# Kernel tuning notes

Hardware: AMD Instinct MI355X
Metric: run time of the kernel (lower is better)

The kernel has to match this reference:

```python
import jax, jax.numpy as jnp
import numpy as np

N_NODES = 100000
N_EDGES = 1200000
D_IN = 64
D_OUT = 32
BN_EPS = 1e-5


def setup_inputs() -> dict:
    key = jax.random.key(0)
    ks = jax.random.split(key, 8)
    x = jax.random.normal(ks[0], (N_NODES, D_IN), dtype=jnp.float32)
    edge_index = jax.random.randint(ks[1], (2, N_EDGES), 0, N_NODES, dtype=jnp.int64)
    W1s = jax.random.normal(ks[2], (3, D_IN, D_IN), dtype=jnp.float32) * 0.05
    b1s = jax.random.normal(ks[3], (3, D_IN), dtype=jnp.float32) * 0.05
    W2s = jax.random.normal(ks[4], (3, D_IN, D_IN), dtype=jnp.float32) * 0.05
    b2s = jax.random.normal(ks[5], (3, D_IN), dtype=jnp.float32) * 0.05
    gammas = jnp.ones((3, D_IN), dtype=jnp.float32)
    betas = jnp.zeros((3, D_IN), dtype=jnp.float32)
    epss = jnp.zeros((3,), dtype=jnp.float32)  # GINConv train_eps init value 0
    lin_w = jax.random.normal(ks[6], (D_IN, D_OUT), dtype=jnp.float32) * 0.05
    lin_b = jnp.zeros((D_OUT,), dtype=jnp.float32)
    return {"x": x, "edge_index": edge_index, "W1s": W1s, "b1s": b1s,
            "W2s": W2s, "b2s": b2s, "gammas": gammas, "betas": betas,
            "epss": epss, "lin_w": lin_w, "lin_b": lin_b}


def reference(x, edge_index, W1s, b1s, W2s, b2s, gammas, betas, epss, lin_w, lin_b):
    # PyG GINConv (source_to_target): out_i = nn((1+eps)*x_i + sum_{j->i} x_j)
    src = edge_index[0]
    dst = edge_index[1]
    n = x.shape[0]
    h = x
    for i in range(3):
        agg = jax.ops.segment_sum(h[src], dst, num_segments=n)  # [N, d]
        z = (1.0 + epss[i]) * h + agg
        z = jax.nn.relu(z @ W1s[i] + b1s[i])
        z = jax.nn.relu(z @ W2s[i] + b2s[i])
        # BatchNorm1d, training mode (batch statistics, biased variance)
        mu = jnp.mean(z, axis=0)
        var = jnp.var(z, axis=0)
        z = gammas[i] * (z - mu) * jax.lax.rsqrt(var + BN_EPS) + betas[i]
        h = jax.nn.relu(z)  # F.relu after each conv
    return h @ lin_w + lin_b  # [N, D_OUT]
```

## Files before the change

### kernel.cpp

```cpp
#include <hip/hip_runtime.h>
#include <hip/hip_fp16.h>

#define NBMAX 256
#define BCAP  8192
#define CHB   3584

typedef _Float16 half8 __attribute__((ext_vector_type(8)));
typedef float f32x4 __attribute__((ext_vector_type(4)));

__device__ __forceinline__ unsigned short f2h(float f) {
    __half h = __float2half_rn(f);
    return *(unsigned short*)&h;
}

__device__ __forceinline__ int scan256(int v, int* wsum, int* woff) {
    int t = threadIdx.x, lane = t & 63, wv = t >> 6;
    int x = v;
    #pragma unroll
    for (int d = 1; d < 64; d <<= 1) {
        int y = __shfl_up(x, d, 64);
        if (lane >= d) x += y;
    }
    if (lane == 63) wsum[wv] = x;
    __syncthreads();
    if (t == 0) {
        int a = 0;
        #pragma unroll
        for (int i = 0; i < 4; ++i) { woff[i] = a; a += wsum[i]; }
    }
    __syncthreads();
    return x - v + woff[wv];
}

__global__ __launch_bounds__(256) void gin_init(const void* __restrict__ edge,
                                                int* __restrict__ flag,
                                                int* __restrict__ gcount, int nb,
                                                float* __restrict__ stats, int E) {
    int t = threadIdx.x;
    for (int i = t; i < nb; i += 256) gcount[i] = 0;
    for (int i = t; i < 384; i += 256) stats[i] = 0.f;
    if (t == 0) {
        const int* p = (const int*)edge;
        int is64 = 1;
        int m = (E < 64) ? E : 64;
        for (int i = 0; i < m; ++i)
            if (p[2 * i + 1] != 0) is64 = 0;
        *flag = is64;
    }
}

__global__ __launch_bounds__(256) void gin_x16(const float* __restrict__ x,
                                               unsigned short* __restrict__ o, int n16) {
    int i = blockIdx.x * 256 + threadIdx.x;
    if (i >= n16) return;
    float4 v = ((const float4*)x)[i];
    ushort4 u;
    u.x = f2h(v.x); u.y = f2h(v.y); u.z = f2h(v.z); u.w = f2h(v.w);
    ((ushort4*)o)[i] = u;
}

__global__ __launch_bounds__(256) void gin_binscatter(const void* __restrict__ edge,
                                                      const int* __restrict__ flag,
                                                      int* __restrict__ gcount,
                                                      uint2* __restrict__ ebuf, int E, int nb) {
    __shared__ int cnt[NBMAX];
    __shared__ int dlt[NBMAX];
    __shared__ int cur[NBMAX];
    __shared__ int wsum[4], woff[4];
    __shared__ uint2 buf[CHB];
    int t = threadIdx.x;
    int beg = blockIdx.x * CHB;
    int m = E - beg; if (m > CHB) m = CHB;
    if (t < nb) cnt[t] = 0;
    __syncthreads();
    int is64 = *flag;
    for (int j = t; j < m; j += 256) {
        int e = beg + j;
        int d = is64 ? (int)((const long long*)edge)[E + e] : ((const int*)edge)[E + e];
        atomicAdd(&cnt[d >> 9], 1);
    }
    __syncthreads();
    int v = (t < nb) ? cnt[t] : 0;
    int excl = scan256(v, wsum, woff);
    if (t < nb) {
        int gb = v ? atomicAdd(&gcount[t], v) : 0;
        dlt[t] = t * BCAP + gb - excl;
        cur[t] = excl;
    }
    __syncthreads();
    for (int j = t; j < m; j += 256) {
        int e = beg + j;
        int s, d;
        if (is64) {
            s = (int)((const long long*)edge)[e];
            d = (int)((const long long*)edge)[E + e];
        } else {
            s = ((const int*)edge)[e];
            d = ((const int*)edge)[E + e];
        }
        int p = atomicAdd(&cur[d >> 9], 1);
        buf[p] = make_uint2((unsigned)s, (unsigned)d);
    }
    __syncthreads();
    for (int j = t; j < m; j += 256) {
        uint2 ed = buf[j];
        ebuf[j + dlt[(int)(ed.y >> 9)]] = ed;
    }
}

__global__ __launch_bounds__(256) void gin_build(const uint2* __restrict__ ebuf,
                                                 const int* __restrict__ gcount,
                                                 int* __restrict__ rowbeg,
                                                 int* __restrict__ rowend,
                                                 int* __restrict__ col, int n) {
    __shared__ int cnt[512];
    __shared__ int off[512];
    __shared__ int wsum[4], woff[4];
    int b = blockIdx.x, t = threadIdx.x;
    int beg = b * BCAP;
    int end = beg + gcount[b];
    cnt[t] = 0; cnt[t + 256] = 0;
    __syncthreads();
    for (int j = beg + t; j < end; j += 256)
        atomicAdd(&cnt[(int)(ebuf[j].y & 511)], 1);
    __syncthreads();
    int v0 = cnt[2 * t], v1 = cnt[2 * t + 1];
    int ep = scan256(v0 + v1, wsum, woff);
    off[2 * t] = ep;
    off[2 * t + 1] = ep + v0;
    __syncthreads();
    int node0 = b * 512 + 2 * t;
    if (node0 < n) {
        rowbeg[node0] = beg + off[2 * t];
        rowend[node0] = beg + off[2 * t] + v0;
    }
    if (node0 + 1 < n) {
        rowbeg[node0 + 1] = beg + off[2 * t + 1];
        rowend[node0 + 1] = beg + off[2 * t + 1] + v1;
    }
    __syncthreads();
    for (int j = beg + t; j < end; j += 256) {
        uint2 ed = ebuf[j];
        int p = atomicAdd(&off[(int)(ed.y & 511)], 1);
        col[beg + p] = (int)ed.x;
    }
}

template <bool APPLY>
__device__ __forceinline__ void accum8(float* acc, uint4 u,
                                       const float* sc, const float* sh) {
    float v[8];
    float2 f;
    f = __half22float2(*(const __half2*)&u.x); v[0] = f.x; v[1] = f.y;
    f = __half22float2(*(const __half2*)&u.y); v[2] = f.x; v[3] = f.y;
    f = __half22float2(*(const __half2*)&u.z); v[4] = f.x; v[5] = f.y;
    f = __half22float2(*(const __half2*)&u.w); v[6] = f.x; v[7] = f.y;
    #pragma unroll
    for (int j = 0; j < 8; ++j)
        acc[j] += APPLY ? fmaxf(fmaf(v[j], sc[j], sh[j]), 0.f) : v[j];
}

template <bool APPLY>
__device__ __forceinline__ void gather_body(const unsigned short* __restrict__ zb,
                                            const int* __restrict__ rowbeg,
                                            const int* __restrict__ rowend,
                                            const int* __restrict__ col,
                                            const float* __restrict__ epss,
                                            const float* __restrict__ ss,
                                            int layer,
                                            unsigned short* __restrict__ t,
                                            int wid, int qn, int l16) {
    int r = l16 >> 3, c = l16 & 7;
    float sc[8] = {1.f, 1.f, 1.f, 1.f, 1.f, 1.f, 1.f, 1.f};
    float sh[8] = {0.f, 0.f, 0.f, 0.f, 0.f, 0.f, 0.f, 0.f};
    if (APPLY) {
        const float* p = ss + (layer - 1) * 128;
        *(float4*)&sc[0] = *(const float4*)(p + 8 * c);
        *(float4*)&sc[4] = *(const float4*)(p + 8 * c + 4);
        *(float4*)&sh[0] = *(const float4*)(p + 64 + 8 * c);
        *(float4*)&sh[4] = *(const float4*)(p + 64 + 8 * c + 4);
    }
    int r0 = rowbeg[wid], r1 = rowend[wid];
    uint4 su = make_uint4(0, 0, 0, 0);
    if (r == 0) su = *(const uint4*)(zb + (size_t)wid * 64 + 8 * c);

    float acc[8] = {0.f, 0.f, 0.f, 0.f, 0.f, 0.f, 0.f, 0.f};
    for (int base = r0; base < r1; base += 16) {
        int ce = base + l16;
        int ci = col[ce < r1 ? ce : r1 - 1];
        uint4 u[8];
        bool p[8];
        #pragma unroll
        for (int s = 0; s < 8; ++s) {
            int j = 2 * s + r;
            p[s] = (base + j) < r1;
            int idx = __shfl(ci, 16 * qn + j);
            if (p[s]) u[s] = *(const uint4*)(zb + (size_t)idx * 64 + 8 * c);
        }
        #pragma unroll
        for (int s = 0; s < 8; ++s)
            if (p[s]) accum8<APPLY>(acc, u[s], sc, sh);
    }
    #pragma unroll
    for (int j = 0; j < 8; ++j)
        acc[j] += __shfl_xor(acc[j], 8);
    if (r == 0) {
        float e1 = 1.f + epss[layer];
        float s[8];
        float2 f;
        f = __half22float2(*(const __half2*)&su.x); s[0] = f.x; s[1] = f.y;
        f = __half22float2(*(const __half2*)&su.y); s[2] = f.x; s[3] = f.y;
        f = __half22float2(*(const __half2*)&su.z); s[4] = f.x; s[5] = f.y;
        f = __half22float2(*(const __half2*)&su.w); s[6] = f.x; s[7] = f.y;
        #pragma unroll
        for (int j = 0; j < 8; ++j) {
            float v = APPLY ? fmaxf(fmaf(s[j], sc[j], sh[j]), 0.f) : s[j];
            acc[j] = fmaf(e1, v, acc[j]);
        }
        uint4 o;
        o.x = (unsigned)f2h(acc[0]) | ((unsigned)f2h(acc[1]) << 16);
        o.y = (unsigned)f2h(acc[2]) | ((unsigned)f2h(acc[3]) << 16);
        o.z = (unsigned)f2h(acc[4]) | ((unsigned)f2h(acc[5]) << 16);
        o.w = (unsigned)f2h(acc[6]) | ((unsigned)f2h(acc[7]) << 16);
        *(uint4*)(t + (size_t)wid * 64 + 8 * c) = o;
    }
}

__global__ __launch_bounds__(256) void gin_gather(const unsigned short* __restrict__ zb,
                                                  const int* __restrict__ rowbeg,
                                                  const int* __restrict__ rowend,
                                                  const int* __restrict__ col,
                                                  const float* __restrict__ epss,
                                                  const float* __restrict__ ss,
                                                  int layer, int apply,
                                                  unsigned short* __restrict__ t, int n) {
    int gw = (blockIdx.x * 256 + threadIdx.x) >> 6;
    int lane = threadIdx.x & 63;
    int qn = lane >> 4;
    int wid = gw * 4 + qn;
    int l16 = lane & 15;
    if (wid >= n) return;
    if (apply)
        gather_body<true>(zb, rowbeg, rowend, col, epss, ss, layer, t, wid, qn, l16);
    else
        gather_body<false>(zb, rowbeg, rowend, col, epss, ss, layer, t, wid, qn, l16);
}

__global__ __launch_bounds__(256) void gin_mlp(const unsigned short* __restrict__ t_in,
                                               unsigned short* __restrict__ z16,
                                               const float* __restrict__ W1g,
                                               const float* __restrict__ b1g,
                                               const float* __restrict__ W2g,
                                               const float* __restrict__ b2g,
                                               float* __restrict__ stats, int layer, int n) {
    __shared__ _Float16 Wt[2 * 64 * 72];
    __shared__ _Float16 Z1[128 * 72];
    __shared__ float sS[64], sQ[64];
    int tid = threadIdx.x;
    int base = blockIdx.x * 128;
    const float* __restrict__ W1 = W1g + layer * 4096;
    const float* __restrict__ W2 = W2g + layer * 4096;

    for (int i = tid; i < 4096; i += 256) {
        int k = i >> 6, nn = i & 63;
        Wt[nn * 72 + k]        = (_Float16)W1[i];
        Wt[4608 + nn * 72 + k] = (_Float16)W2[i];
    }
    if (tid < 64) { sS[tid] = 0.f; sQ[tid] = 0.f; }
    __syncthreads();

    int lane = tid & 63, wv = tid >> 6;
    int g = lane >> 4, q = lane & 15;
    int n0 = 32 * wv + q;
    int n1 = n0 + 16;

    const _Float16* tp = (const _Float16*)t_in + (size_t)base * 64;
    half8 tb00 = *(const half8*)(tp + (size_t)n0 * 64 + 8 * g);
    half8 tb01 = *(const half8*)(tp + (size_t)n0 * 64 + 32 + 8 * g);
    half8 tb10 = *(const half8*)(tp + (size_t)n1 * 64 + 8 * g);
    half8 tb11 = *(const half8*)(tp + (size_t)n1 * 64 + 32 + 8 * g);

    f32x4 acc[2][4];
    #pragma unroll
    for (int nt = 0; nt < 2; ++nt)
        #pragma unroll
        for (int ft = 0; ft < 4; ++ft)
            acc[nt][ft] = (f32x4){0.f, 0.f, 0.f, 0.f};

    #pragma unroll
    for (int ft = 0; ft < 4; ++ft) {
        half8 a0 = *(const half8*)&Wt[(16 * ft + q) * 72 + 8 * g];
        half8 a1 = *(const half8*)&Wt[(16 * ft + q) * 72 + 32 + 8 * g];
        acc[0][ft] = __builtin_amdgcn_mfma_f32_16x16x32_f16(a0, tb00, acc[0][ft], 0, 0, 0);
        acc[0][ft] = __builtin_amdgcn_mfma_f32_16x16x32_f16(a1, tb01, acc[0][ft], 0, 0, 0);
        acc[1][ft] = __builtin_amdgcn_mfma_f32_16x16x32_f16(a0, tb10, acc[1][ft], 0, 0, 0);
        acc[1][ft] = __builtin_amdgcn_mfma_f32_16x16x32_f16(a1, tb11, acc[1][ft], 0, 0, 0);
    }

    #pragma unroll
    for (int ft = 0; ft < 4; ++ft) {
        float4 b = *(const float4*)(b1g + layer * 64 + 16 * ft + 4 * g);
        #pragma unroll
        for (int nt = 0; nt < 2; ++nt) {
            int node = nt ? n1 : n0;
            float v0 = fmaxf(acc[nt][ft][0] + b.x, 0.f);
            float v1 = fmaxf(acc[nt][ft][1] + b.y, 0.f);
            float v2 = fmaxf(acc[nt][ft][2] + b.z, 0.f);
            float v3 = fmaxf(acc[nt][ft][3] + b.w, 0.f);
            uint2 pk;
            pk.x = (unsigned)f2h(v0) | ((unsigned)f2h(v1) << 16);
            pk.y = (unsigned)f2h(v2) | ((unsigned)f2h(v3) << 16);
            *(uint2*)&Z1[node * 72 + 16 * ft + 4 * g] = pk;
        }
    }

    half8 zb00 = *(const half8*)&Z1[n0 * 72 + 8 * g];
    half8 zb01 = *(const half8*)&Z1[n0 * 72 + 32 + 8 * g];
    half8 zb10 = *(const half8*)&Z1[n1 * 72 + 8 * g];
    half8 zb11 = *(const half8*)&Z1[n1 * 72 + 32 + 8 * g];
    #pragma unroll
    for (int nt = 0; nt < 2; ++nt)
        #pragma unroll
        for (int ft = 0; ft < 4; ++ft)
            acc[nt][ft] = (f32x4){0.f, 0.f, 0.f, 0.f};
    #pragma unroll
    for (int ft = 0; ft < 4; ++ft) {
        half8 a0 = *(const half8*)&Wt[4608 + (16 * ft + q) * 72 + 8 * g];
        half8 a1 = *(const half8*)&Wt[4608 + (16 * ft + q) * 72 + 32 + 8 * g];
        acc[0][ft] = __builtin_amdgcn_mfma_f32_16x16x32_f16(a0, zb00, acc[0][ft], 0, 0, 0);
        acc[0][ft] = __builtin_amdgcn_mfma_f32_16x16x32_f16(a1, zb01, acc[0][ft], 0, 0, 0);
        acc[1][ft] = __builtin_amdgcn_mfma_f32_16x16x32_f16(a0, zb10, acc[1][ft], 0, 0, 0);
        acc[1][ft] = __builtin_amdgcn_mfma_f32_16x16x32_f16(a1, zb11, acc[1][ft], 0, 0, 0);
    }

    #pragma unroll
    for (int ft = 0; ft < 4; ++ft) {
        float4 b = *(const float4*)(b2g + layer * 64 + 16 * ft + 4 * g);
        float s[4] = {0.f, 0.f, 0.f, 0.f};
        float sq[4] = {0.f, 0.f, 0.f, 0.f};
        #pragma unroll
        for (int nt = 0; nt < 2; ++nt) {
            int node = base + (nt ? n1 : n0);
            float v0 = fmaxf(acc[nt][ft][0] + b.x, 0.f);
            float v1 = fmaxf(acc[nt][ft][1] + b.y, 0.f);
            float v2 = fmaxf(acc[nt][ft][2] + b.z, 0.f);
            float v3 = fmaxf(acc[nt][ft][3] + b.w, 0.f);
            if (node < n) {
                s[0] += v0; sq[0] += v0 * v0;
                s[1] += v1; sq[1] += v1 * v1;
                s[2] += v2; sq[2] += v2 * v2;
                s[3] += v3; sq[3] += v3 * v3;
                uint2 pk;
                pk.x = (unsigned)f2h(v0) | ((unsigned)f2h(v1) << 16);
                pk.y = (unsigned)f2h(v2) | ((unsigned)f2h(v3) << 16);
                *(uint2*)(z16 + (size_t)node * 64 + 16 * ft + 4 * g) = pk;
            }
        }
        #pragma unroll
        for (int off = 1; off < 16; off <<= 1) {
            #pragma unroll
            for (int r2 = 0; r2 < 4; ++r2) {
                s[r2] += __shfl_xor(s[r2], off);
                sq[r2] += __shfl_xor(sq[r2], off);
            }
        }
        if (q == 0) {
            #pragma unroll
            for (int r2 = 0; r2 < 4; ++r2) {
                atomicAdd(&sS[16 * ft + 4 * g + r2], s[r2]);
                atomicAdd(&sQ[16 * ft + 4 * g + r2], sq[r2]);
            }
        }
    }
    __syncthreads();
    if (tid < 64) {
        atomicAdd(&stats[layer * 128 + tid], sS[tid]);
        atomicAdd(&stats[layer * 128 + 64 + tid], sQ[tid]);
    }
}

__global__ void gin_bnfin(const float* __restrict__ stats, const float* __restrict__ gammas,
                          const float* __restrict__ betas, float* __restrict__ ss,
                          int layer, float n) {
    int f = threadIdx.x;
    float mu = stats[layer * 128 + f] / n;
    float var = stats[layer * 128 + 64 + f] / n - mu * mu;
    float rs = rsqrtf(var + 1e-5f);
    float g = gammas[layer * 64 + f];
    float b = betas[layer * 64 + f];
    ss[layer * 128 + f] = g * rs;
    ss[layer * 128 + 64 + f] = b - g * rs * mu;
}

__global__ __launch_bounds__(256) void gin_lin(const unsigned short* __restrict__ zin,
                                               const float* __restrict__ stats,
                                               const float* __restrict__ gammas,
                                               const float* __restrict__ betas,
                                               float fN,
                                               const float* __restrict__ lw,
                                               const float* __restrict__ lb,
                                               float* __restrict__ out, int n) {
    __shared__ float Z[128 * 68];
    int tid = threadIdx.x;
    int base = blockIdx.x * 128;
    int cq = (tid & 15) * 4;
    float4 sc4, sh4;
    {
        float t0[4], t1[4];
        #pragma unroll
        for (int j = 0; j < 4; ++j) {
            int f = cq + j;
            float mu  = stats[256 + f] / fN;
            float var = stats[256 + 64 + f] / fN - mu * mu;
            float g   = gammas[128 + f];
            float grs = g * rsqrtf(var + 1e-5f);
            t0[j] = grs;
            t1[j] = betas[128 + f] - grs * mu;
        }
        sc4 = make_float4(t0[0], t0[1], t0[2], t0[3]);
        sh4 = make_float4(t1[0], t1[1], t1[2], t1[3]);
    }
    {
        const ushort4* __restrict__ src = (const ushort4*)(zin + (size_t)base * 64);
        #pragma unroll
        for (int it = 0; it < 8; ++it) {
            int idx4 = it * 256 + tid;
            int row = idx4 >> 4, c = (idx4 & 15) * 4;
            float4 v = make_float4(0.f, 0.f, 0.f, 0.f);
            if (base + row < n) {
                ushort4 u = src[idx4];
                float2 f0 = __half22float2(*(const __half2*)&u.x);
                float2 f1 = __half22float2(*(const __half2*)&u.z);
                v = make_float4(f0.x, f0.y, f1.x, f1.y);
            }
            float4 r;
            r.x = fmaxf(fmaf(v.x, sc4.x, sh4.x), 0.f);
            r.y = fmaxf(fmaf(v.y, sc4.y, sh4.y), 0.f);
            r.z = fmaxf(fmaf(v.z, sc4.z, sh4.z), 0.f);
            r.w = fmaxf(fmaf(v.w, sc4.w, sh4.w), 0.f);
            *(float4*)&Z[row * 68 + c] = r;
        }
    }
    __syncthreads();
    int tx = tid & 7, ty = tid >> 3;
    float acc[4][4];
    {
        float4 b = *(const float4*)(lb + 4 * tx);
        #pragma unroll
        for (int r = 0; r < 4; ++r) {
            acc[r][0] = b.x; acc[r][1] = b.y; acc[r][2] = b.z; acc[r][3] = b.w;
        }
    }
    #pragma unroll 4
    for (int k = 0; k < 64; ++k) {
        float4 w = *(const float4*)(lw + k * 32 + 4 * tx);
        #pragma unroll
        for (int r = 0; r < 4; ++r) {
            float a = Z[(ty + 32 * r) * 68 + k];
            acc[r][0] = fmaf(a, w.x, acc[r][0]);
            acc[r][1] = fmaf(a, w.y, acc[r][1]);
            acc[r][2] = fmaf(a, w.z, acc[r][2]);
            acc[r][3] = fmaf(a, w.w, acc[r][3]);
        }
    }
    #pragma unroll
    for (int r = 0; r < 4; ++r) {
        int row = base + ty + 32 * r;
        if (row < n) {
            float4 v;
            v.x = acc[r][0]; v.y = acc[r][1]; v.z = acc[r][2]; v.w = acc[r][3];
            *(float4*)(out + (size_t)row * 32 + 4 * tx) = v;
        }
    }
}

extern "C" void kernel_launch(void* const* d_in, const int* in_sizes, int n_in,
                              void* d_out, int out_size, void* d_ws, size_t ws_size,
                              hipStream_t stream) {
    const float* x      = (const float*)d_in[0];
    const void*  edge   = d_in[1];
    const float* W1s    = (const float*)d_in[2];
    const float* b1s    = (const float*)d_in[3];
    const float* W2s    = (const float*)d_in[4];
    const float* b2s    = (const float*)d_in[5];
    const float* gammas = (const float*)d_in[6];
    const float* betas  = (const float*)d_in[7];
    const float* epss   = (const float*)d_in[8];
    const float* lin_w  = (const float*)d_in[9];
    const float* lin_b  = (const float*)d_in[10];
    float* out = (float*)d_out;

    const int N = in_sizes[0] / 64;
    const int E = in_sizes[1] / 2;
    const int NB = (N + 511) >> 9;
    const float fN = (float)N;

    char* w = (char*)d_ws;
    auto take = [&](size_t bytes) {
        char* p = w;
        w += (bytes + 255) & ~(size_t)255;
        return p;
    };
    unsigned short* x16 = (unsigned short*)take((size_t)N * 64 * 2);
    unsigned short* hA  = (unsigned short*)take((size_t)N * 64 * 2);
    unsigned short* hB  = (unsigned short*)take((size_t)N * 64 * 2);
    unsigned short* T   = (unsigned short*)take((size_t)N * 64 * 2);
    uint2* ebuf    = (uint2*)take((size_t)NB * BCAP * 8);
    int*   col     = (int*)take((size_t)NB * BCAP * 4);
    int*   rowbeg  = (int*)take((size_t)N * 4);
    int*   rowend  = (int*)take((size_t)N * 4);
    int*   gcount  = (int*)take((size_t)NBMAX * 4);
    float* stats   = (float*)take(3 * 128 * 4);
    float* ss      = (float*)take(3 * 128 * 4);
    int*   flag    = (int*)take(4);

    gin_init<<<1, 256, 0, stream>>>(edge, flag, gcount, NB, stats, E);
    gin_x16<<<(N * 16 + 255) / 256, 256, 0, stream>>>(x, x16, N * 16);
    gin_binscatter<<<(E + CHB - 1) / CHB, 256, 0, stream>>>(edge, flag, gcount, ebuf, E, NB);
    gin_build<<<NB, 256, 0, stream>>>(ebuf, gcount, rowbeg, rowend, col, N);

    const int gGather = (N + 15) / 16;
    const int gMlp    = (N + 127) / 128;

    const unsigned short* zin = x16;
    unsigned short* zout = hA;
    for (int L = 0; L < 3; ++L) {
        gin_gather<<<gGather, 256, 0, stream>>>(zin, rowbeg, rowend, col, epss, ss, L,
                                                (L > 0) ? 1 : 0, T, N);
        gin_mlp<<<gMlp, 256, 0, stream>>>(T, zout, W1s, b1s, W2s, b2s, stats, L, N);
        if (L < 2) gin_bnfin<<<1, 64, 0, stream>>>(stats, gammas, betas, ss, L, fN);
        zin = zout;
        zout = (zout == hA) ? hB : hA;
    }
    gin_lin<<<gMlp, 256, 0, stream>>>(zin, stats, gammas, betas, fN, lin_w, lin_b, out, N);
}
```

Measured before the change: 324.0 us.

## Fuse neighbor gather into MLP kernel and fold BN finalize and init

Merges the per-layer gather kernel into the MLP kernel so aggregated rows go straight into shared memory instead of a global T buffer, and computes the BN scale/shift per block from stats, which removes the bnfin launches. The init kernel is folded into the x-to-fp16 conversion as an extra block. This removes a global write and read of N×64 fp16 per layer plus several launches. In exchange, each 128-node block does its gather sequentially across 8 passes, giving less gather parallelism per block and possibly lower occupancy from the larger fused kernel.

```diff
diff --git a/kernel.cpp b/kernel.cpp
--- a/kernel.cpp
+++ b/kernel.cpp
@@ -32,25 +32,26 @@
     return x - v + woff[wv];
 }
 
-__global__ __launch_bounds__(256) void gin_init(const void* __restrict__ edge,
-                                                int* __restrict__ flag,
-                                                int* __restrict__ gcount, int nb,
-                                                float* __restrict__ stats, int E) {
-    int t = threadIdx.x;
-    for (int i = t; i < nb; i += 256) gcount[i] = 0;
-    for (int i = t; i < 384; i += 256) stats[i] = 0.f;
-    if (t == 0) {
-        const int* p = (const int*)edge;
-        int is64 = 1;
-        int m = (E < 64) ? E : 64;
-        for (int i = 0; i < m; ++i)
-            if (p[2 * i + 1] != 0) is64 = 0;
-        *flag = is64;
-    }
-}
-
-__global__ __launch_bounds__(256) void gin_x16(const float* __restrict__ x,
-                                               unsigned short* __restrict__ o, int n16) {
+__global__ __launch_bounds__(256) void gin_x16init(const float* __restrict__ x,
+                                                   unsigned short* __restrict__ o, int n16,
+                                                   const void* __restrict__ edge,
+                                                   int* __restrict__ flag,
+                                                   int* __restrict__ gcount, int nb,
+                                                   float* __restrict__ stats, int E) {
+    if (blockIdx.x == gridDim.x - 1) {
+        int t = threadIdx.x;
+        for (int i = t; i < nb; i += 256) gcount[i] = 0;
+        for (int i = t; i < 384; i += 256) stats[i] = 0.f;
+        if (t == 0) {
+            const int* p = (const int*)edge;
+            int is64 = 1;
+            int m = (E < 64) ? E : 64;
+            for (int i = 0; i < m; ++i)
+                if (p[2 * i + 1] != 0) is64 = 0;
+            *flag = is64;
+        }
+        return;
+    }
     int i = blockIdx.x * 256 + threadIdx.x;
     if (i >= n16) return;
     float4 v = ((const float4*)x)[i];
@@ -161,39 +162,27 @@
 }
 
 template <bool APPLY>
-__device__ __forceinline__ void gather_body(const unsigned short* __restrict__ zb,
-                                            const int* __restrict__ rowbeg,
-                                            const int* __restrict__ rowend,
+__device__ __forceinline__ void gather_node(const unsigned short* __restrict__ zb,
+                                            int r0, int r1,
                                             const int* __restrict__ col,
-                                            const float* __restrict__ epss,
-                                            const float* __restrict__ ss,
-                                            int layer,
-                                            unsigned short* __restrict__ t,
+                                            float e1,
+                                            const float* sc, const float* sh,
+                                            _Float16* __restrict__ trow,
                                             int wid, int qn, int l16) {
     int r = l16 >> 3, c = l16 & 7;
-    float sc[8] = {1.f, 1.f, 1.f, 1.f, 1.f, 1.f, 1.f, 1.f};
-    float sh[8] = {0.f, 0.f, 0.f, 0.f, 0.f, 0.f, 0.f, 0.f};
-    if (APPLY) {
-        const float* p = ss + (layer - 1) * 128;
-        *(float4*)&sc[0] = *(const float4*)(p + 8 * c);
-        *(float4*)&sc[4] = *(const float4*)(p + 8 * c + 4);
-        *(float4*)&sh[0] = *(const float4*)(p + 64 + 8 * c);
-        *(float4*)&sh[4] = *(const float4*)(p + 64 + 8 * c + 4);
-    }
-    int r0 = rowbeg[wid], r1 = rowend[wid];
     uint4 su = make_uint4(0, 0, 0, 0);
     if (r == 0) su = *(const uint4*)(zb + (size_t)wid * 64 + 8 * c);
 
     float acc[8] = {0.f, 0.f, 0.f, 0.f, 0.f, 0.f, 0.f, 0.f};
-    for (int base = r0; base < r1; base += 16) {
-        int ce = base + l16;
+    for (int b2 = r0; b2 < r1; b2 += 16) {
+        int ce = b2 + l16;
         int ci = col[ce < r1 ? ce : r1 - 1];
         uint4 u[8];
         bool p[8];
         #pragma unroll
         for (int s = 0; s < 8; ++s) {
             int j = 2 * s + r;
-            p[s] = (base + j) < r1;
+            p[s] = (b2 + j) < r1;
             int idx = __shfl(ci, 16 * qn + j);
             if (p[s]) u[s] = *(const uint4*)(zb + (size_t)idx * 64 + 8 * c);
         }
@@ -205,7 +194,6 @@
     for (int j = 0; j < 8; ++j)
         acc[j] += __shfl_xor(acc[j], 8);
     if (r == 0) {
-        float e1 = 1.f + epss[layer];
         float s[8];
         float2 f;
         f = __half22float2(*(const __half2*)&su.x); s[0] = f.x; s[1] = f.y;
@@ -222,40 +210,30 @@
         o.y = (unsigned)f2h(acc[2]) | ((unsigned)f2h(acc[3]) << 16);
         o.z = (unsigned)f2h(acc[4]) | ((unsigned)f2h(acc[5]) << 16);
         o.w = (unsigned)f2h(acc[6]) | ((unsigned)f2h(acc[7]) << 16);
-        *(uint4*)(t + (size_t)wid * 64 + 8 * c) = o;
-    }
-}
-
-__global__ __launch_bounds__(256) void gin_gather(const unsigned short* __restrict__ zb,
-                                                  const int* __restrict__ rowbeg,
-                                                  const int* __restrict__ rowend,
-                                                  const int* __restrict__ col,
-                                                  const float* __restrict__ epss,
-                                                  const float* __restrict__ ss,
-                                                  int layer, int apply,
-                                                  unsigned short* __restrict__ t, int n) {
-    int gw = (blockIdx.x * 256 + threadIdx.x) >> 6;
-    int lane = threadIdx.x & 63;
-    int qn = lane >> 4;
-    int wid = gw * 4 + qn;
-    int l16 = lane & 15;
-    if (wid >= n) return;
-    if (apply)
-        gather_body<true>(zb, rowbeg, rowend, col, epss, ss, layer, t, wid, qn, l16);
-    else
-        gather_body<false>(zb, rowbeg, rowend, col, epss, ss, layer, t, wid, qn, l16);
-}
-
-__global__ __launch_bounds__(256) void gin_mlp(const unsigned short* __restrict__ t_in,
-                                               unsigned short* __restrict__ z16,
-                                               const float* __restrict__ W1g,
-                                               const float* __restrict__ b1g,
-                                               const float* __restrict__ W2g,
-                                               const float* __restrict__ b2g,
-                                               float* __restrict__ stats, int layer, int n) {
+        *(uint4*)(trow + 8 * c) = o;
+    }
+}
+
+template <bool APPLY>
+__global__ __launch_bounds__(256, 4) void gin_fused(const unsigned short* __restrict__ zb,
+                                                    const int* __restrict__ rowbeg,
+                                                    const int* __restrict__ rowend,
+                                                    const int* __restrict__ col,
+                                                    const float* __restrict__ epss,
+                                                    const float* __restrict__ gammas,
+                                                    const float* __restrict__ betas,
+                                                    float fN,
+                                                    unsigned short* __restrict__ z16,
+                                                    const float* __restrict__ W1g,
+                                                    const float* __restrict__ b1g,
+                                                    const float* __restrict__ W2g,
+                                                    const float* __restrict__ b2g,
+                                                    float* __restrict__ stats,
+                                                    int layer, int n) {
     __shared__ _Float16 Wt[2 * 64 * 72];
-    __shared__ _Float16 Z1[128 * 72];
+    __shared__ _Float16 Tz[128 * 72];
     __shared__ float sS[64], sQ[64];
+    __shared__ float sBN[128];
     int tid = threadIdx.x;
     int base = blockIdx.x * 128;
     const float* __restrict__ W1 = W1g + layer * 4096;
@@ -266,19 +244,63 @@
         Wt[nn * 72 + k]        = (_Float16)W1[i];
         Wt[4608 + nn * 72 + k] = (_Float16)W2[i];
     }
-    if (tid < 64) { sS[tid] = 0.f; sQ[tid] = 0.f; }
+    if (tid < 64) {
+        sS[tid] = 0.f; sQ[tid] = 0.f;
+        if (APPLY) {
+            float mu  = stats[(layer - 1) * 128 + tid] / fN;
+            float var = stats[(layer - 1) * 128 + 64 + tid] / fN - mu * mu;
+            float g   = gammas[(layer - 1) * 64 + tid];
+            float grs = g * rsqrtf(var + 1e-5f);
+            sBN[tid]      = grs;
+            sBN[64 + tid] = betas[(layer - 1) * 64 + tid] - grs * mu;
+        }
+    }
     __syncthreads();
 
     int lane = tid & 63, wv = tid >> 6;
-    int g = lane >> 4, q = lane & 15;
+    int qn = lane >> 4;
+    int l16 = lane & 15;
+    int c8 = l16 & 7;
+    float e1 = 1.f + epss[layer];
+    float sc[8] = {1.f, 1.f, 1.f, 1.f, 1.f, 1.f, 1.f, 1.f};
+    float sh[8] = {0.f, 0.f, 0.f, 0.f, 0.f, 0.f, 0.f, 0.f};
+    if (APPLY) {
+        *(float4*)&sc[0] = *(const float4*)&sBN[8 * c8];
+        *(float4*)&sc[4] = *(const float4*)&sBN[8 * c8 + 4];
+        *(float4*)&sh[0] = *(const float4*)&sBN[64 + 8 * c8];
+        *(float4*)&sh[4] = *(const float4*)&sBN[64 + 8 * c8 + 4];
+    }
+
+    int wid0 = base + wv * 4 + qn;
+    int nr0 = 0, nr1 = 0;
+    if (wid0 < n) { nr0 = rowbeg[wid0]; nr1 = rowend[wid0]; }
+    #pragma unroll 1
+    for (int p = 0; p < 8; ++p) {
+        int widl = p * 16 + wv * 4 + qn;
+        int wid = base + widl;
+        int r0 = nr0, r1 = nr1;
+        if (p < 7) {
+            int w2 = wid + 16;
+            nr0 = 0; nr1 = 0;
+            if (w2 < n) { nr0 = rowbeg[w2]; nr1 = rowend[w2]; }
+        }
+        if (wid < n) {
+            gather_node<APPLY>(zb, r0, r1, col, e1, sc, sh,
+                               Tz + widl * 72, wid, qn, l16);
+        } else if (l16 < 8) {
+            *(uint4*)(Tz + widl * 72 + 8 * c8) = make_uint4(0u, 0u, 0u, 0u);
+        }
+    }
+    __syncthreads();
+
+    int g = qn, q = l16;
     int n0 = 32 * wv + q;
     int n1 = n0 + 16;
 
-    const _Float16* tp = (const _Float16*)t_in + (size_t)base * 64;
-    half8 tb00 = *(const half8*)(tp + (size_t)n0 * 64 + 8 * g);
-    half8 tb01 = *(const half8*)(tp + (size_t)n0 * 64 + 32 + 8 * g);
-    half8 tb10 = *(const half8*)(tp + (size_t)n1 * 64 + 8 * g);
-    half8 tb11 = *(const half8*)(tp + (size_t)n1 * 64 + 32 + 8 * g);
+    half8 tb00 = *(const half8*)&Tz[n0 * 72 + 8 * g];
+    half8 tb01 = *(const half8*)&Tz[n0 * 72 + 32 + 8 * g];
+    half8 tb10 = *(const half8*)&Tz[n1 * 72 + 8 * g];
+    half8 tb11 = *(const half8*)&Tz[n1 * 72 + 32 + 8 * g];
 
     f32x4 acc[2][4];
     #pragma unroll
@@ -310,14 +332,14 @@
             uint2 pk;
             pk.x = (unsigned)f2h(v0) | ((unsigned)f2h(v1) << 16);
             pk.y = (unsigned)f2h(v2) | ((unsigned)f2h(v3) << 16);
-            *(uint2*)&Z1[node * 72 + 16 * ft + 4 * g] = pk;
-        }
-    }
-
-    half8 zb00 = *(const half8*)&Z1[n0 * 72 + 8 * g];
-    half8 zb01 = *(const half8*)&Z1[n0 * 72 + 32 + 8 * g];
-    half8 zb10 = *(const half8*)&Z1[n1 * 72 + 8 * g];
-    half8 zb11 = *(const half8*)&Z1[n1 * 72 + 32 + 8 * g];
+            *(uint2*)&Tz[node * 72 + 16 * ft + 4 * g] = pk;
+        }
+    }
+
+    half8 zb00 = *(const half8*)&Tz[n0 * 72 + 8 * g];
+    half8 zb01 = *(const half8*)&Tz[n0 * 72 + 32 + 8 * g];
+    half8 zb10 = *(const half8*)&Tz[n1 * 72 + 8 * g];
+    half8 zb11 = *(const half8*)&Tz[n1 * 72 + 32 + 8 * g];
     #pragma unroll
     for (int nt = 0; nt < 2; ++nt)
         #pragma unroll
@@ -379,19 +401,6 @@
     }
 }
 
-__global__ void gin_bnfin(const float* __restrict__ stats, const float* __restrict__ gammas,
-                          const float* __restrict__ betas, float* __restrict__ ss,
-                          int layer, float n) {
-    int f = threadIdx.x;
-    float mu = stats[layer * 128 + f] / n;
-    float var = stats[layer * 128 + 64 + f] / n - mu * mu;
-    float rs = rsqrtf(var + 1e-5f);
-    float g = gammas[layer * 64 + f];
-    float b = betas[layer * 64 + f];
-    ss[layer * 128 + f] = g * rs;
-    ss[layer * 128 + 64 + f] = b - g * rs * mu;
-}
-
 __global__ __launch_bounds__(256) void gin_lin(const unsigned short* __restrict__ zin,
                                                const float* __restrict__ stats,
                                                const float* __restrict__ gammas,
@@ -504,31 +513,32 @@
     unsigned short* x16 = (unsigned short*)take((size_t)N * 64 * 2);
     unsigned short* hA  = (unsigned short*)take((size_t)N * 64 * 2);
     unsigned short* hB  = (unsigned short*)take((size_t)N * 64 * 2);
-    unsigned short* T   = (unsigned short*)take((size_t)N * 64 * 2);
     uint2* ebuf    = (uint2*)take((size_t)NB * BCAP * 8);
     int*   col     = (int*)take((size_t)NB * BCAP * 4);
     int*   rowbeg  = (int*)take((size_t)N * 4);
     int*   rowend  = (int*)take((size_t)N * 4);
     int*   gcount  = (int*)take((size_t)NBMAX * 4);
     float* stats   = (float*)take(3 * 128 * 4);
-    float* ss      = (float*)take(3 * 128 * 4);
     int*   flag    = (int*)take(4);
 
-    gin_init<<<1, 256, 0, stream>>>(edge, flag, gcount, NB, stats, E);
-    gin_x16<<<(N * 16 + 255) / 256, 256, 0, stream>>>(x, x16, N * 16);
+    const int n16 = N * 16;
+    gin_x16init<<<(n16 + 255) / 256 + 1, 256, 0, stream>>>(x, x16, n16, edge, flag,
+                                                           gcount, NB, stats, E);
     gin_binscatter<<<(E + CHB - 1) / CHB, 256, 0, stream>>>(edge, flag, gcount, ebuf, E, NB);
     gin_build<<<NB, 256, 0, stream>>>(ebuf, gcount, rowbeg, rowend, col, N);
 
-    const int gGather = (N + 15) / 16;
-    const int gMlp    = (N + 127) / 128;
-
+    const int gMlp = (N + 127) / 128;
     const unsigned short* zin = x16;
     unsigned short* zout = hA;
     for (int L = 0; L < 3; ++L) {
-        gin_gather<<<gGather, 256, 0, stream>>>(zin, rowbeg, rowend, col, epss, ss, L,
-                                                (L > 0) ? 1 : 0, T, N);
-        gin_mlp<<<gMlp, 256, 0, stream>>>(T, zout, W1s, b1s, W2s, b2s, stats, L, N);
-        if (L < 2) gin_bnfin<<<1, 64, 0, stream>>>(stats, gammas, betas, ss, L, fN);
+        if (L == 0)
+            gin_fused<false><<<gMlp, 256, 0, stream>>>(zin, rowbeg, rowend, col, epss,
+                                                       gammas, betas, fN, zout,
+                                                       W1s, b1s, W2s, b2s, stats, L, N);
+        else
+            gin_fused<true><<<gMlp, 256, 0, stream>>>(zin, rowbeg, rowend, col, epss,
+                                                      gammas, betas, fN, zout,
+                                                      W1s, b1s, W2s, b2s, stats, L, N);
         zin = zout;
         zout = (zout == hA) ? hB : hA;
     }
```

Result: faster. 294.7 us (-9.0%).
